# Performance work log

Hardware: AMD Instinct MI355X
Metric: run time of the kernel (lower is better)

The kernel has to match this reference:

```python
import jax, jax.numpy as jnp
import numpy as np

K_NEIGHBORS = 16
HEADS = 4
BN_EPS = 1e-5


def _bn(x, p):
    # eval-mode BatchNorm; p is [4, C] = (gamma, beta, running_mean, running_var), x is [..., C]
    g, b, m, v = p[0], p[1], p[2], p[3]
    return (x - m) * (g / jnp.sqrt(v + BN_EPS)) + b


def setup_inputs() -> dict:
    key = jax.random.key(0)
    ks = jax.random.split(key, 16)
    B, C, H, W = 4, 192, 32, 32
    Hd = 384  # hidden_channels

    def bn_params(k, c):
        k1, k2, k3, k4 = jax.random.split(k, 4)
        gamma = 1.0 + 0.1 * jax.random.normal(k1, (c,), jnp.float32)
        beta = 0.1 * jax.random.normal(k2, (c,), jnp.float32)
        mean = 0.1 * jax.random.normal(k3, (c,), jnp.float32)
        var = jax.random.uniform(k4, (c,), jnp.float32, 0.5, 1.5)
        return jnp.stack([gamma, beta, mean, var])

    x = jax.random.normal(ks[0], (B, C, H, W), jnp.float32)
    W1 = 0.05 * jax.random.normal(ks[1], (C, C), jnp.float32)          # fc1 1x1 conv [out,in]
    b1 = 0.02 * jax.random.normal(ks[2], (C,), jnp.float32)
    bn1 = bn_params(ks[3], C)
    Wg = 0.05 * jax.random.normal(ks[4], (C, HEADS * Hd), jnp.float32)  # GATConv shared lin
    att_src = 0.1 * jax.random.normal(ks[5], (HEADS, Hd), jnp.float32)
    att_dst = 0.1 * jax.random.normal(ks[6], (HEADS, Hd), jnp.float32)
    bg = 0.02 * jax.random.normal(ks[7], (Hd,), jnp.float32)            # GATConv bias (concat=False)
    bng = bn_params(ks[8], Hd)
    W2 = 0.05 * jax.random.normal(ks[9], (C, Hd), jnp.float32)          # fc2 1x1 conv [out,in]
    b2 = 0.02 * jax.random.normal(ks[10], (C,), jnp.float32)
    bn2 = bn_params(ks[11], C)
    return {"x": x, "W1": W1, "b1": b1, "bn1": bn1, "Wg": Wg,
            "att_src": att_src, "att_dst": att_dst, "bg": bg, "bng": bng,
            "W2": W2, "b2": b2, "bn2": bn2}


def reference(x, W1, b1, bn1, Wg, att_src, att_dst, bg, bng, W2, b2, bn2):
    B, C, H, W = x.shape
    N = H * W
    Hd = Wg.shape[1] // HEADS
    xf = x.reshape(B, C, N).transpose(0, 2, 1)          # [B,N,C] node features
    shortcut = xf

    # fc1: 1x1 conv + BN
    y = _bn(xf @ W1.T + b1, bn1)                        # [B,N,C]

    # dynamic KNN graph per image (loop=True -> self included, distance 0)
    sq = jnp.sum(y * y, axis=-1)                        # [B,N]
    dist = sq[:, :, None] + sq[:, None, :] - 2.0 * jnp.einsum('bnc,bmc->bnm', y, y)
    idx = jax.lax.top_k(-dist, K_NEIGHBORS)[1]          # [B,N,k] neighbor (source) ids
    bidx = jnp.arange(B)[:, None, None]

    # GATConv (shared lin, heads=4, concat=False -> mean over heads)
    h = (y @ Wg).reshape(B, N, HEADS, Hd)               # [B,N,h,d]
    a_src = jnp.sum(h * att_src, axis=-1)               # [B,N,h]
    a_dst = jnp.sum(h * att_dst, axis=-1)               # [B,N,h]
    e = jax.nn.leaky_relu(a_src[bidx, idx] + a_dst[:, :, None, :], 0.2)  # [B,N,k,h]
    attn = jax.nn.softmax(e, axis=2)                    # softmax over the k incoming edges
    h_nbr = h[bidx, idx]                                # [B,N,k,h,d] gathered neighbor feats
    g = jnp.einsum('bnkh,bnkhd->bnhd', attn, h_nbr).mean(axis=2) + bg  # [B,N,Hd]

    g = jax.nn.gelu(_bn(g, bng), approximate=False)

    # fc2: 1x1 conv + BN, residual
    out = _bn(g @ W2.T + b2, bn2) + shortcut            # [B,N,C]
    return out.transpose(0, 2, 1).reshape(B, C, H, W)
```

## Files before the change

### kernel.cpp

```cpp
#include <hip/hip_runtime.h>
#include <math.h>

#define Bb 4
#define Cc 192
#define NN 1024
#define HD 384
#define NH 4
#define FF 1536
#define KN 16
#define BN_EPS 1e-5f

typedef __attribute__((ext_vector_type(8))) short bf16x8;
typedef __attribute__((ext_vector_type(4))) float f32x4;

__device__ inline float b2f(ushort u) {
  return __uint_as_float(((unsigned)u) << 16);
}
__device__ inline ushort f2b(float f) {
  unsigned v = __float_as_uint(f);
  return (ushort)((v + 0x7fffu + ((v >> 16) & 1u)) >> 16);
}

#define FMA_ROW(ACC, AV, B) \
  ACC.x = fmaf(AV, B.x, ACC.x); ACC.y = fmaf(AV, B.y, ACC.y); \
  ACC.z = fmaf(AV, B.z, ACC.z); ACC.w = fmaf(AV, B.w, ACC.w);

__global__ __launch_bounds__(256) void k_prep(
    const float* __restrict__ W1, const float* __restrict__ W2,
    const float* __restrict__ Wg, float* __restrict__ W1T,
    float* __restrict__ W2T, ushort* __restrict__ WgTb) {
  __shared__ float tile[32][33];
  int id = blockIdx.x;
  const float* in; int R, C, cx, cy;
  float* outf = nullptr; ushort* outb = nullptr;
  if (id < 36)       { in = W1; R = Cc; C = Cc;   cx = id % 6;        cy = id / 6;        outf = W1T; }
  else if (id < 108) { int q = id - 36;  in = W2; R = Cc; C = HD;  cx = q % 12; cy = q / 12; outf = W2T; }
  else               { int q = id - 108; in = Wg; R = Cc; C = FF;  cx = q % 48; cy = q / 48; outb = WgTb; }
  int c0 = cx * 32, r0 = cy * 32;
  int tx = threadIdx.x & 31, ty = threadIdx.x >> 5;
#pragma unroll
  for (int i = 0; i < 4; ++i) {
    int r = ty + i * 8;
    tile[r][tx] = in[(size_t)(r0 + r) * C + c0 + tx];
  }
  __syncthreads();
#pragma unroll
  for (int i = 0; i < 4; ++i) {
    int r = ty + i * 8;
    float v = tile[tx][r];
    if (outf) outf[(size_t)(c0 + r) * R + r0 + tx] = v;
    else      outb[(size_t)(c0 + r) * R + r0 + tx] = f2b(v);
  }
}

__global__ __launch_bounds__(256) void k_fc1(
    const float* __restrict__ x, const float* __restrict__ W1T,
    const float* __restrict__ b1, const float* __restrict__ bn1,
    float* __restrict__ y, ushort* __restrict__ yb) {
  int nt = blockIdx.x, ct = blockIdx.y, b = blockIdx.z;
  int n0 = nt * 64, ct64 = ct * 64;
  __shared__ float As[64][64];
  __shared__ float Bs[64][64];
  int t = threadIdx.x;
  int tx = t & 15, ty = t >> 4;
  float4 acc[4];
#pragma unroll
  for (int i = 0; i < 4; ++i) acc[i] = {0.f, 0.f, 0.f, 0.f};
  for (int k0 = 0; k0 < Cc; k0 += 64) {
    __syncthreads();
#pragma unroll
    for (int i = 0; i < 4; ++i) {
      int fi = i * 256 + t;
      int r = fi >> 4, q = fi & 15;
      *(float4*)&As[r][q * 4] =
          *(const float4*)&x[((size_t)b * Cc + k0 + r) * NN + n0 + q * 4];
      *(float4*)&Bs[r][q * 4] =
          *(const float4*)&W1T[(size_t)(k0 + r) * Cc + ct64 + q * 4];
    }
    __syncthreads();
#pragma unroll 8
    for (int k = 0; k < 64; ++k) {
      float4 a = *(const float4*)&As[k][ty * 4];
      float4 bv = *(const float4*)&Bs[k][tx * 4];
      FMA_ROW(acc[0], a.x, bv)
      FMA_ROW(acc[1], a.y, bv)
      FMA_ROW(acc[2], a.z, bv)
      FMA_ROW(acc[3], a.w, bv)
    }
  }
  float s[4], mm[4], be[4], bias[4];
#pragma unroll
  for (int jj = 0; jj < 4; ++jj) {
    int c = ct64 + tx * 4 + jj;
    s[jj]    = bn1[c] / sqrtf(bn1[3 * Cc + c] + BN_EPS);
    mm[jj]   = bn1[2 * Cc + c];
    be[jj]   = bn1[Cc + c];
    bias[jj] = b1[c];
  }
  float accm[4][4] = {
      {acc[0].x, acc[0].y, acc[0].z, acc[0].w},
      {acc[1].x, acc[1].y, acc[1].z, acc[1].w},
      {acc[2].x, acc[2].y, acc[2].z, acc[2].w},
      {acc[3].x, acc[3].y, acc[3].z, acc[3].w}};
#pragma unroll
  for (int ii = 0; ii < 4; ++ii) {
    int n = n0 + ty * 4 + ii;
    float4 o;
    o.x = (accm[ii][0] + bias[0] - mm[0]) * s[0] + be[0];
    o.y = (accm[ii][1] + bias[1] - mm[1]) * s[1] + be[1];
    o.z = (accm[ii][2] + bias[2] - mm[2]) * s[2] + be[2];
    o.w = (accm[ii][3] + bias[3] - mm[3]) * s[3] + be[3];
    *(float4*)&y[((size_t)b * NN + n) * Cc + ct64 + tx * 4] = o;
    ushort4 ob = {f2b(o.x), f2b(o.y), f2b(o.z), f2b(o.w)};
    *(ushort4*)&yb[((size_t)b * NN + n) * Cc + ct64 + tx * 4] = ob;
  }
}

__global__ __launch_bounds__(256) void k_tr(const float* __restrict__ in,
                                            float* __restrict__ out,
                                            int R, int C) {
  __shared__ float tile[32][33];
  int c0 = blockIdx.x * 32, r0 = blockIdx.y * 32;
  const float* ip = in + (size_t)blockIdx.z * R * C;
  float* op = out + (size_t)blockIdx.z * R * C;
  int tx = threadIdx.x & 31, ty = threadIdx.x >> 5;
#pragma unroll
  for (int i = 0; i < 4; ++i) {
    int r = ty + i * 8;
    tile[r][tx] = ip[(size_t)(r0 + r) * C + c0 + tx];
  }
  __syncthreads();
#pragma unroll
  for (int i = 0; i < 4; ++i) {
    int r = ty + i * 8;
    op[(size_t)(c0 + r) * R + r0 + tx] = tile[tx][r];
  }
}

__global__ __launch_bounds__(64) void k_sq(const float* __restrict__ y,
                                           float* __restrict__ sq) {
  int bn = blockIdx.x;
  int lane = threadIdx.x;
  const float* yp = y + (size_t)bn * Cc;
  float s = 0.f;
  for (int k = lane; k < Cc; k += 64) { float v = yp[k]; s = fmaf(v, v, s); }
#pragma unroll
  for (int off = 32; off; off >>= 1) s += __shfl_down(s, off);
  if (lane == 0) sq[bn] = s;
}

__global__ __launch_bounds__(256) void k_hgemm_mfma(
    const ushort* __restrict__ yb, const ushort* __restrict__ WgTb,
    ushort* __restrict__ hb) {
  int r0 = blockIdx.x * 128, c0 = blockIdx.y * 128;
  __shared__ ushort Al[128][72];
  __shared__ ushort Bl[128][72];
  int t = threadIdx.x;
  int w = t >> 6, l = t & 63;
  int wr = w >> 1, wc = w & 1;
  f32x4 acc[4][4];
#pragma unroll
  for (int mt = 0; mt < 4; ++mt)
#pragma unroll
    for (int nt = 0; nt < 4; ++nt) acc[mt][nt] = {0.f, 0.f, 0.f, 0.f};
  for (int k0 = 0; k0 < Cc; k0 += 64) {
    __syncthreads();
#pragma unroll
    for (int i = 0; i < 4; ++i) {
      int u = i * 256 + t;
      int r = u >> 3, ko = (u & 7) * 8;
      *(int4*)&Al[r][ko] = *(const int4*)&yb[(size_t)(r0 + r) * Cc + k0 + ko];
      *(int4*)&Bl[r][ko] = *(const int4*)&WgTb[(size_t)(c0 + r) * Cc + k0 + ko];
    }
    __syncthreads();
#pragma unroll
    for (int ks = 0; ks < 2; ++ks) {
      bf16x8 af[4], bfr[4];
#pragma unroll
      for (int mt = 0; mt < 4; ++mt)
        af[mt] = *(const bf16x8*)&Al[wr * 64 + mt * 16 + (l & 15)][ks * 32 + (l >> 4) * 8];
#pragma unroll
      for (int nt = 0; nt < 4; ++nt)
        bfr[nt] = *(const bf16x8*)&Bl[wc * 64 + nt * 16 + (l & 15)][ks * 32 + (l >> 4) * 8];
#pragma unroll
      for (int mt = 0; mt < 4; ++mt)
#pragma unroll
        for (int nt = 0; nt < 4; ++nt)
          acc[mt][nt] = __builtin_amdgcn_mfma_f32_16x16x32_bf16(
              af[mt], bfr[nt], acc[mt][nt], 0, 0, 0);
    }
  }
  int col_l = l & 15, rg = l >> 4;
#pragma unroll
  for (int mt = 0; mt < 4; ++mt)
#pragma unroll
    for (int nt = 0; nt < 4; ++nt) {
      int col = c0 + wc * 64 + nt * 16 + col_l;
#pragma unroll
      for (int j = 0; j < 4; ++j) {
        int row = r0 + wr * 64 + mt * 16 + rg * 4 + j;
        hb[(size_t)row * FF + col] = f2b(acc[mt][nt][j]);
      }
    }
}

__global__ __launch_bounds__(256) void k_attn_coef(
    const ushort* __restrict__ hb, const float* __restrict__ att_src,
    const float* __restrict__ att_dst, float* __restrict__ asrc,
    float* __restrict__ adst) {
  int bn = blockIdx.x;
  int head = threadIdx.x / 64, lane = threadIdx.x % 64;
  const ushort* hp = hb + (size_t)bn * FF + head * HD;
  const float* as = att_src + head * HD;
  const float* ad = att_dst + head * HD;
  float s1 = 0.f, s2 = 0.f;
  for (int d = lane; d < HD; d += 64) {
    float v = b2f(hp[d]);
    s1 = fmaf(v, as[d], s1);
    s2 = fmaf(v, ad[d], s2);
  }
#pragma unroll
  for (int off = 32; off; off >>= 1) {
    s1 += __shfl_down(s1, off);
    s2 += __shfl_down(s2, off);
  }
  if (lane == 0) {
    asrc[bn * NH + head] = s1;
    adst[bn * NH + head] = s2;
  }
}

__global__ __launch_bounds__(256) void k_dist(const float* __restrict__ yT,
                                              const float* __restrict__ sq,
                                              float* __restrict__ dist) {
  int b = blockIdx.z;
  int n0 = blockIdx.y * 128, m0 = blockIdx.x * 64;
  __shared__ float As[64][128];
  __shared__ float Bs[64][64];
  const float* ytb = yT + (size_t)b * Cc * NN;
  int t = threadIdx.x;
  int tx = t & 15, ty = t >> 4;
  float4 acc[8];
#pragma unroll
  for (int i = 0; i < 8; ++i) acc[i] = {0.f, 0.f, 0.f, 0.f};
  for (int k0 = 0; k0 < Cc; k0 += 64) {
    __syncthreads();
#pragma unroll
    for (int i = 0; i < 8; ++i) {
      int fi = i * 256 + t;
      int kk = fi >> 5, n4 = fi & 31;
      *(float4*)&As[kk][n4 * 4] =
          *(const float4*)&ytb[(size_t)(k0 + kk) * NN + n0 + n4 * 4];
    }
#pragma unroll
    for (int i = 0; i < 4; ++i) {
      int fi = i * 256 + t;
      int kk = fi >> 4, m4 = fi & 15;
      *(float4*)&Bs[kk][m4 * 4] =
          *(const float4*)&ytb[(size_t)(k0 + kk) * NN + m0 + m4 * 4];
    }
    __syncthreads();
#pragma unroll 8
    for (int k = 0; k < 64; ++k) {
      float4 a0 = *(const float4*)&As[k][ty * 4];
      float4 a1 = *(const float4*)&As[k][64 + ty * 4];
      float4 b4 = *(const float4*)&Bs[k][tx * 4];
      FMA_ROW(acc[0], a0.x, b4)
      FMA_ROW(acc[1], a0.y, b4)
      FMA_ROW(acc[2], a0.z, b4)
      FMA_ROW(acc[3], a0.w, b4)
      FMA_ROW(acc[4], a1.x, b4)
      FMA_ROW(acc[5], a1.y, b4)
      FMA_ROW(acc[6], a1.z, b4)
      FMA_ROW(acc[7], a1.w, b4)
    }
  }
#pragma unroll
  for (int ii = 0; ii < 8; ++ii) {
    int n = n0 + ((ii < 4) ? (ty * 4 + ii) : (64 + ty * 4 + ii - 4));
    float sn = sq[b * NN + n];
    int mbase = m0 + tx * 4;
    float av[4] = {acc[ii].x, acc[ii].y, acc[ii].z, acc[ii].w};
    float4 o;
    o.x = sn + sq[b * NN + mbase + 0] - 2.f * av[0];
    o.y = sn + sq[b * NN + mbase + 1] - 2.f * av[1];
    o.z = sn + sq[b * NN + mbase + 2] - 2.f * av[2];
    o.w = sn + sq[b * NN + mbase + 3] - 2.f * av[3];
    *(float4*)&dist[((size_t)b * NN + n) * NN + mbase] = o;
  }
}

__global__ __launch_bounds__(64) void k_topk(const float* __restrict__ dist,
                                             int* __restrict__ idx) {
  int bn = blockIdx.x;
  int lane = threadIdx.x;
  const float4* dp = (const float4*)(dist + (size_t)bn * NN);
  float dv[16];
#pragma unroll
  for (int q = 0; q < 4; ++q) {
    float4 v = dp[lane + 64 * q];
    dv[q * 4 + 0] = v.x; dv[q * 4 + 1] = v.y;
    dv[q * 4 + 2] = v.z; dv[q * 4 + 3] = v.w;
  }
  for (int sel = 0; sel < KN; ++sel) {
    float bv = INFINITY;
    int bi = 0x7fffffff;
#pragma unroll
    for (int q = 0; q < 4; ++q)
#pragma unroll
      for (int j = 0; j < 4; ++j) {
        int m = (lane + 64 * q) * 4 + j;
        float v = dv[q * 4 + j];
        if (v < bv || (v == bv && m < bi)) { bv = v; bi = m; }
      }
#pragma unroll
    for (int off = 32; off; off >>= 1) {
      float ov = __shfl_xor(bv, off);
      int oi   = __shfl_xor(bi, off);
      if (ov < bv || (ov == bv && oi < bi)) { bv = ov; bi = oi; }
    }
    if (lane == 0) idx[bn * KN + sel] = bi;
#pragma unroll
    for (int q = 0; q < 4; ++q)
#pragma unroll
      for (int j = 0; j < 4; ++j)
        if ((lane + 64 * q) * 4 + j == bi) dv[q * 4 + j] = INFINITY;
  }
}

__global__ __launch_bounds__(128, 4) void k_gat(
    const ushort* __restrict__ hb, const float* __restrict__ asrc,
    const float* __restrict__ adst, const int* __restrict__ idx,
    const float* __restrict__ bg, const float* __restrict__ bng,
    float* __restrict__ g) {
  int bid = blockIdx.x;
  int bn = (bid & 7) * (Bb * NN / 8) + (bid >> 3);
  int b = bn / NN;
  __shared__ int nb[KN];
  __shared__ float attn[KN][NH];
  int t = threadIdx.x;
  if (t < KN) nb[t] = idx[bn * KN + t];
  __syncthreads();
  if (t < KN * NH) {
    int k = t % KN, hd = t / KN;
    float e = asrc[((size_t)b * NN + nb[k]) * NH + hd] +
              adst[(size_t)bn * NH + hd];
    e = (e >= 0.f) ? e : 0.2f * e;
    attn[k][hd] = e;
  }
  __syncthreads();
  if (t < NH) {
    float mx = -INFINITY;
    for (int k = 0; k < KN; ++k) mx = fmaxf(mx, attn[k][t]);
    float s = 0.f;
    for (int k = 0; k < KN; ++k) {
      float ev = expf(attn[k][t] - mx);
      attn[k][t] = ev;
      s += ev;
    }
    float inv = 1.f / s;
    for (int k = 0; k < KN; ++k) attn[k][t] *= inv;
  }
  __syncthreads();
  if (t < 96) {
    int d = t * 4;
    float4 acc = {0.f, 0.f, 0.f, 0.f};
#pragma unroll 4
    for (int k = 0; k < KN; ++k) {
      const ushort* hp = hb + ((size_t)b * NN + nb[k]) * FF + d;
      float4 aw = *(const float4*)&attn[k][0];
      ushort4 u0 = *(const ushort4*)&hp[0];
      ushort4 u1 = *(const ushort4*)&hp[HD];
      ushort4 u2 = *(const ushort4*)&hp[2 * HD];
      ushort4 u3 = *(const ushort4*)&hp[3 * HD];
      float4 h0 = {b2f(u0.x), b2f(u0.y), b2f(u0.z), b2f(u0.w)};
      float4 h1 = {b2f(u1.x), b2f(u1.y), b2f(u1.z), b2f(u1.w)};
      float4 h2 = {b2f(u2.x), b2f(u2.y), b2f(u2.z), b2f(u2.w)};
      float4 h3 = {b2f(u3.x), b2f(u3.y), b2f(u3.z), b2f(u3.w)};
      acc.x = fmaf(aw.x, h0.x, acc.x); acc.x = fmaf(aw.y, h1.x, acc.x);
      acc.x = fmaf(aw.z, h2.x, acc.x); acc.x = fmaf(aw.w, h3.x, acc.x);
      acc.y = fmaf(aw.x, h0.y, acc.y); acc.y = fmaf(aw.y, h1.y, acc.y);
      acc.y = fmaf(aw.z, h2.y, acc.y); acc.y = fmaf(aw.w, h3.y, acc.y);
      acc.z = fmaf(aw.x, h0.z, acc.z); acc.z = fmaf(aw.y, h1.z, acc.z);
      acc.z = fmaf(aw.z, h2.z, acc.z); acc.z = fmaf(aw.w, h3.z, acc.z);
      acc.w = fmaf(aw.x, h0.w, acc.w); acc.w = fmaf(aw.y, h1.w, acc.w);
      acc.w = fmaf(aw.z, h2.w, acc.w); acc.w = fmaf(aw.w, h3.w, acc.w);
    }
    float o[4] = {acc.x, acc.y, acc.z, acc.w};
    float4 r;
    float* rp = (float*)&r;
#pragma unroll
    for (int j = 0; j < 4; ++j) {
      int dd = d + j;
      float val = o[j] * 0.25f + bg[dd];
      float sc = bng[dd] / sqrtf(bng[3 * HD + dd] + BN_EPS);
      val = (val - bng[2 * HD + dd]) * sc + bng[HD + dd];
      val = 0.5f * val * (1.f + erff(val * 0.7071067811865475f));
      rp[j] = val;
    }
    *(float4*)&g[(size_t)bn * HD + d] = r;
  }
}

__global__ __launch_bounds__(256) void k_fc2(
    const float* __restrict__ gT, const float* __restrict__ W2T,
    const float* __restrict__ b2, const float* __restrict__ bn2,
    const float* __restrict__ x, float* __restrict__ out) {
  int nt = blockIdx.x, ct = blockIdx.y, b = blockIdx.z;
  int n0 = nt * 64, c0 = ct * 64;
  __shared__ float As[64][64];
  __shared__ float Bs[64][64];
  int t = threadIdx.x;
  int tx = t & 15, ty = t >> 4;
  float4 acc[4];
#pragma unroll
  for (int i = 0; i < 4; ++i) acc[i] = {0.f, 0.f, 0.f, 0.f};
  for (int k0 = 0; k0 < HD; k0 += 64) {
    __syncthreads();
#pragma unroll
    for (int i = 0; i < 4; ++i) {
      int fi = i * 256 + t;
      int r = fi >> 4, q = fi & 15;
      *(float4*)&As[r][q * 4] =
          *(const float4*)&gT[((size_t)b * HD + k0 + r) * NN + n0 + q * 4];
      *(float4*)&Bs[r][q * 4] =
          *(const float4*)&W2T[(size_t)(k0 + r) * Cc + c0 + q * 4];
    }
    __syncthreads();
#pragma unroll 8
    for (int k = 0; k < 64; ++k) {
      float4 a = *(const float4*)&As[k][ty * 4];
      float4 bv = *(const float4*)&Bs[k][tx * 4];
      FMA_ROW(acc[0], a.x, bv)
      FMA_ROW(acc[1], a.y, bv)
      FMA_ROW(acc[2], a.z, bv)
      FMA_ROW(acc[3], a.w, bv)
    }
  }
  float accm[4][4] = {
      {acc[0].x, acc[0].y, acc[0].z, acc[0].w},
      {acc[1].x, acc[1].y, acc[1].z, acc[1].w},
      {acc[2].x, acc[2].y, acc[2].z, acc[2].w},
      {acc[3].x, acc[3].y, acc[3].z, acc[3].w}};
#pragma unroll
  for (int jj = 0; jj < 4; ++jj) {
    int c = c0 + tx * 4 + jj;
    float s  = bn2[c] / sqrtf(bn2[3 * Cc + c] + BN_EPS);
    float mm = bn2[2 * Cc + c];
    float be = bn2[Cc + c];
    float bias = b2[c];
    float4 res = *(const float4*)&x[((size_t)b * Cc + c) * NN + n0 + ty * 4];
    float4 o;
    o.x = (accm[0][jj] + bias - mm) * s + be + res.x;
    o.y = (accm[1][jj] + bias - mm) * s + be + res.y;
    o.z = (accm[2][jj] + bias - mm) * s + be + res.z;
    o.w = (accm[3][jj] + bias - mm) * s + be + res.w;
    *(float4*)&out[((size_t)b * Cc + c) * NN + n0 + ty * 4] = o;
  }
}

extern "C" void kernel_launch(void* const* d_in, const int* in_sizes, int n_in,
                              void* d_out, int out_size, void* d_ws, size_t ws_size,
                              hipStream_t stream) {
  const float* x       = (const float*)d_in[0];
  const float* W1      = (const float*)d_in[1];
  const float* b1      = (const float*)d_in[2];
  const float* bn1     = (const float*)d_in[3];
  const float* Wg      = (const float*)d_in[4];
  const float* att_src = (const float*)d_in[5];
  const float* att_dst = (const float*)d_in[6];
  const float* bg      = (const float*)d_in[7];
  const float* bng     = (const float*)d_in[8];
  const float* W2      = (const float*)d_in[9];
  const float* b2      = (const float*)d_in[10];
  const float* bn2     = (const float*)d_in[11];
  float* out = (float*)d_out;

  float* ws    = (float*)d_ws;
  float* y     = ws;
  float* sq    = y + 786432;
  float* asrc  = sq + 4096;
  float* adst  = asrc + 16384;
  float* dist  = adst + 16384;
  float* g     = dist;
  int*   idx   = (int*)(dist + 4194304);
  float* yT    = dist + 4194304 + 65536;
  float* gT    = yT + 786432;
  float* W1T   = gT + 1572864;
  float* W2T   = W1T + 36864;
  ushort* yb   = (ushort*)(W2T + 73728);
  ushort* WgTb = (ushort*)(W2T + 73728 + 393216);
  ushort* hb   = (ushort*)(W2T + 73728 + 393216 + 147456);

  k_prep<<<396, 256, 0, stream>>>(W1, W2, Wg, W1T, W2T, WgTb);
  k_fc1<<<dim3(16, 3, 4), 256, 0, stream>>>(x, W1T, b1, bn1, y, yb);
  k_tr<<<dim3(6, 32, 4), 256, 0, stream>>>(y, yT, NN, Cc);
  k_sq<<<Bb * NN, 64, 0, stream>>>(y, sq);
  k_hgemm_mfma<<<dim3(32, 12), 256, 0, stream>>>(yb, WgTb, hb);
  k_attn_coef<<<Bb * NN, 256, 0, stream>>>(hb, att_src, att_dst, asrc, adst);
  k_dist<<<dim3(16, 8, 4), 256, 0, stream>>>(yT, sq, dist);
  k_topk<<<Bb * NN, 64, 0, stream>>>(dist, idx);
  k_gat<<<Bb * NN, 128, 0, stream>>>(hb, asrc, adst, idx, bg, bng, g);
  k_tr<<<dim3(12, 32, 4), 256, 0, stream>>>(g, gT, NN, HD);
  k_fc2<<<dim3(16, 3, 4), 256, 0, stream>>>(gT, W2T, b2, bn2, x, out);
}
```

Measured before the change: 148.2 us.

## Fold attention vectors into weights, run fc2 on MFMA, drop g transpose

New measurement: 160.4 us. +8.2%, slower.

```diff
diff --git a/kernel.cpp b/kernel.cpp
--- a/kernel.cpp
+++ b/kernel.cpp
@@ -27,29 +27,47 @@
 
 __global__ __launch_bounds__(256) void k_prep(
     const float* __restrict__ W1, const float* __restrict__ W2,
-    const float* __restrict__ Wg, float* __restrict__ W1T,
-    float* __restrict__ W2T, ushort* __restrict__ WgTb) {
+    const float* __restrict__ Wg, const float* __restrict__ att_src,
+    const float* __restrict__ att_dst, float* __restrict__ W1T,
+    ushort* __restrict__ W2b, ushort* __restrict__ WgTb,
+    float* __restrict__ Asml) {
   __shared__ float tile[32][33];
   int id = blockIdx.x;
-  const float* in; int R, C, cx, cy;
-  float* outf = nullptr; ushort* outb = nullptr;
-  if (id < 36)       { in = W1; R = Cc; C = Cc;   cx = id % 6;        cy = id / 6;        outf = W1T; }
-  else if (id < 108) { int q = id - 36;  in = W2; R = Cc; C = HD;  cx = q % 12; cy = q / 12; outf = W2T; }
-  else               { int q = id - 108; in = Wg; R = Cc; C = FF;  cx = q % 48; cy = q / 48; outb = WgTb; }
-  int c0 = cx * 32, r0 = cy * 32;
-  int tx = threadIdx.x & 31, ty = threadIdx.x >> 5;
-#pragma unroll
-  for (int i = 0; i < 4; ++i) {
-    int r = ty + i * 8;
-    tile[r][tx] = in[(size_t)(r0 + r) * C + c0 + tx];
-  }
-  __syncthreads();
-#pragma unroll
-  for (int i = 0; i < 4; ++i) {
-    int r = ty + i * 8;
-    float v = tile[tx][r];
-    if (outf) outf[(size_t)(c0 + r) * R + r0 + tx] = v;
-    else      outb[(size_t)(c0 + r) * R + r0 + tx] = f2b(v);
+  int t = threadIdx.x;
+  if (id < 36 || (id >= 108 && id < 396)) {
+    const float* in; int R, C, cx, cy;
+    float* outf = nullptr; ushort* outb = nullptr;
+    if (id < 36) { in = W1; R = Cc; C = Cc; cx = id % 6; cy = id / 6; outf = W1T; }
+    else { int q = id - 108; in = Wg; R = Cc; C = FF; cx = q % 48; cy = q / 48; outb = WgTb; }
+    int c0 = cx * 32, r0 = cy * 32;
+    int tx = t & 31, ty = t >> 5;
+#pragma unroll
+    for (int i = 0; i < 4; ++i) {
+      int r = ty + i * 8;
+      tile[r][tx] = in[(size_t)(r0 + r) * C + c0 + tx];
+    }
+    __syncthreads();
+#pragma unroll
+    for (int i = 0; i < 4; ++i) {
+      int r = ty + i * 8;
+      float v = tile[tx][r];
+      if (outf) outf[(size_t)(c0 + r) * R + r0 + tx] = v;
+      else      outb[(size_t)(c0 + r) * R + r0 + tx] = f2b(v);
+    }
+  } else if (id < 108) {
+    int base = (id - 36) * 1024 + t * 4;
+    float4 v = *(const float4*)&W2[base];
+    ushort4 o = {f2b(v.x), f2b(v.y), f2b(v.z), f2b(v.w)};
+    *(ushort4*)&W2b[base] = o;
+  } else {
+    int gi = (id - 396) * 256 + t;
+    int k = gi >> 3, j = gi & 7;
+    int h = j & 3;
+    const float* av = (j < 4) ? att_src : att_dst;
+    float acc = 0.f;
+    for (int d = 0; d < HD; ++d)
+      acc = fmaf(Wg[(size_t)k * FF + h * HD + d], av[h * HD + d], acc);
+    Asml[k * 8 + j] = acc;
   }
 }
 
@@ -204,30 +222,25 @@
     }
 }
 
-__global__ __launch_bounds__(256) void k_attn_coef(
-    const ushort* __restrict__ hb, const float* __restrict__ att_src,
-    const float* __restrict__ att_dst, float* __restrict__ asrc,
-    float* __restrict__ adst) {
-  int bn = blockIdx.x;
-  int head = threadIdx.x / 64, lane = threadIdx.x % 64;
-  const ushort* hp = hb + (size_t)bn * FF + head * HD;
-  const float* as = att_src + head * HD;
-  const float* ad = att_dst + head * HD;
-  float s1 = 0.f, s2 = 0.f;
-  for (int d = lane; d < HD; d += 64) {
-    float v = b2f(hp[d]);
-    s1 = fmaf(v, as[d], s1);
-    s2 = fmaf(v, ad[d], s2);
-  }
-#pragma unroll
-  for (int off = 32; off; off >>= 1) {
-    s1 += __shfl_down(s1, off);
-    s2 += __shfl_down(s2, off);
-  }
-  if (lane == 0) {
-    asrc[bn * NH + head] = s1;
-    adst[bn * NH + head] = s2;
-  }
+__global__ __launch_bounds__(256) void k_attn2(
+    const float* __restrict__ yT, const float* __restrict__ Asml,
+    float* __restrict__ asrc, float* __restrict__ adst) {
+  __shared__ float As[Cc][8];
+  int t = threadIdx.x;
+  for (int i = t; i < Cc * 8; i += 256) As[i >> 3][i & 7] = Asml[i];
+  int blk = blockIdx.x;
+  int b = blk >> 5;
+  int n0 = (blk & 31) * 32;
+  int nl = t & 31, j = t >> 5;
+  __syncthreads();
+  const float* yp = yT + (size_t)b * Cc * NN + n0 + nl;
+  float acc = 0.f;
+#pragma unroll 4
+  for (int k = 0; k < Cc; ++k)
+    acc = fmaf(yp[(size_t)k * NN], As[k][j], acc);
+  int bn = b * NN + n0 + nl;
+  if (j < 4) asrc[bn * NH + j] = acc;
+  else       adst[bn * NH + (j - 4)] = acc;
 }
 
 __global__ __launch_bounds__(256) void k_dist(const float* __restrict__ yT,
@@ -332,7 +345,7 @@
     const ushort* __restrict__ hb, const float* __restrict__ asrc,
     const float* __restrict__ adst, const int* __restrict__ idx,
     const float* __restrict__ bg, const float* __restrict__ bng,
-    float* __restrict__ g) {
+    ushort* __restrict__ gb) {
   int bid = blockIdx.x;
   int bn = (bid & 7) * (Bb * NN / 8) + (bid >> 3);
   int b = bn / NN;
@@ -387,8 +400,8 @@
       acc.w = fmaf(aw.z, h2.w, acc.w); acc.w = fmaf(aw.w, h3.w, acc.w);
     }
     float o[4] = {acc.x, acc.y, acc.z, acc.w};
-    float4 r;
-    float* rp = (float*)&r;
+    ushort4 r;
+    ushort* rp = (ushort*)&r;
 #pragma unroll
     for (int j = 0; j < 4; ++j) {
       int dd = d + j;
@@ -396,66 +409,88 @@
       float sc = bng[dd] / sqrtf(bng[3 * HD + dd] + BN_EPS);
       val = (val - bng[2 * HD + dd]) * sc + bng[HD + dd];
       val = 0.5f * val * (1.f + erff(val * 0.7071067811865475f));
-      rp[j] = val;
-    }
-    *(float4*)&g[(size_t)bn * HD + d] = r;
-  }
-}
-
-__global__ __launch_bounds__(256) void k_fc2(
-    const float* __restrict__ gT, const float* __restrict__ W2T,
+      rp[j] = f2b(val);
+    }
+    *(ushort4*)&gb[(size_t)bn * HD + d] = r;
+  }
+}
+
+__global__ __launch_bounds__(256) void k_fc2_mfma(
+    const ushort* __restrict__ gb, const ushort* __restrict__ W2b,
     const float* __restrict__ b2, const float* __restrict__ bn2,
     const float* __restrict__ x, float* __restrict__ out) {
-  int nt = blockIdx.x, ct = blockIdx.y, b = blockIdx.z;
-  int n0 = nt * 64, c0 = ct * 64;
-  __shared__ float As[64][64];
-  __shared__ float Bs[64][64];
-  int t = threadIdx.x;
-  int tx = t & 15, ty = t >> 4;
-  float4 acc[4];
-#pragma unroll
-  for (int i = 0; i < 4; ++i) acc[i] = {0.f, 0.f, 0.f, 0.f};
+  int r0 = blockIdx.x * 64;
+  int c0 = blockIdx.y * 64;
+  int b = r0 >> 10, n0 = r0 & 1023;
+  __shared__ ushort smem[2 * 64 * 72];
+  ushort* Al = smem;
+  ushort* Bl = smem + 64 * 72;
+  int t = threadIdx.x;
+  int w = t >> 6, l = t & 63;
+  int wr = w >> 1, wc = w & 1;
+  f32x4 acc[2][2];
+#pragma unroll
+  for (int mt = 0; mt < 2; ++mt)
+#pragma unroll
+    for (int nt = 0; nt < 2; ++nt) acc[mt][nt] = {0.f, 0.f, 0.f, 0.f};
   for (int k0 = 0; k0 < HD; k0 += 64) {
     __syncthreads();
 #pragma unroll
-    for (int i = 0; i < 4; ++i) {
-      int fi = i * 256 + t;
-      int r = fi >> 4, q = fi & 15;
-      *(float4*)&As[r][q * 4] =
-          *(const float4*)&gT[((size_t)b * HD + k0 + r) * NN + n0 + q * 4];
-      *(float4*)&Bs[r][q * 4] =
-          *(const float4*)&W2T[(size_t)(k0 + r) * Cc + c0 + q * 4];
-    }
-    __syncthreads();
-#pragma unroll 8
-    for (int k = 0; k < 64; ++k) {
-      float4 a = *(const float4*)&As[k][ty * 4];
-      float4 bv = *(const float4*)&Bs[k][tx * 4];
-      FMA_ROW(acc[0], a.x, bv)
-      FMA_ROW(acc[1], a.y, bv)
-      FMA_ROW(acc[2], a.z, bv)
-      FMA_ROW(acc[3], a.w, bv)
-    }
-  }
-  float accm[4][4] = {
-      {acc[0].x, acc[0].y, acc[0].z, acc[0].w},
-      {acc[1].x, acc[1].y, acc[1].z, acc[1].w},
-      {acc[2].x, acc[2].y, acc[2].z, acc[2].w},
-      {acc[3].x, acc[3].y, acc[3].z, acc[3].w}};
-#pragma unroll
-  for (int jj = 0; jj < 4; ++jj) {
-    int c = c0 + tx * 4 + jj;
+    for (int i = 0; i < 2; ++i) {
+      int u = i * 256 + t;
+      int r = u >> 3, ko = (u & 7) * 8;
+      *(int4*)&Al[r * 72 + ko] = *(const int4*)&gb[(size_t)(r0 + r) * HD + k0 + ko];
+      *(int4*)&Bl[r * 72 + ko] = *(const int4*)&W2b[(size_t)(c0 + r) * HD + k0 + ko];
+    }
+    __syncthreads();
+#pragma unroll
+    for (int ks = 0; ks < 2; ++ks) {
+      bf16x8 af[2], bfr[2];
+#pragma unroll
+      for (int mt = 0; mt < 2; ++mt)
+        af[mt] = *(const bf16x8*)&Al[(wr * 32 + mt * 16 + (l & 15)) * 72 + ks * 32 + (l >> 4) * 8];
+#pragma unroll
+      for (int nt = 0; nt < 2; ++nt)
+        bfr[nt] = *(const bf16x8*)&Bl[(wc * 32 + nt * 16 + (l & 15)) * 72 + ks * 32 + (l >> 4) * 8];
+#pragma unroll
+      for (int mt = 0; mt < 2; ++mt)
+#pragma unroll
+        for (int nt = 0; nt < 2; ++nt)
+          acc[mt][nt] = __builtin_amdgcn_mfma_f32_16x16x32_bf16(
+              af[mt], bfr[nt], acc[mt][nt], 0, 0, 0);
+    }
+  }
+  __syncthreads();
+  float* ct = (float*)smem;
+  int col_l = l & 15, rg = l >> 4;
+#pragma unroll
+  for (int mt = 0; mt < 2; ++mt)
+#pragma unroll
+    for (int nt = 0; nt < 2; ++nt) {
+      int cl = wc * 32 + nt * 16 + col_l;
+      int nl = wr * 32 + mt * 16 + rg * 4;
+      float4 v = {acc[mt][nt][0], acc[mt][nt][1], acc[mt][nt][2], acc[mt][nt][3]};
+      *(float4*)&ct[cl * 68 + nl] = v;
+    }
+  __syncthreads();
+#pragma unroll
+  for (int i = 0; i < 4; ++i) {
+    int u = i * 256 + t;
+    int cl = u >> 4, q = u & 15;
+    float4 v = *(const float4*)&ct[cl * 68 + q * 4];
+    int c = c0 + cl;
     float s  = bn2[c] / sqrtf(bn2[3 * Cc + c] + BN_EPS);
     float mm = bn2[2 * Cc + c];
     float be = bn2[Cc + c];
     float bias = b2[c];
-    float4 res = *(const float4*)&x[((size_t)b * Cc + c) * NN + n0 + ty * 4];
+    size_t base = ((size_t)b * Cc + c) * NN + n0 + q * 4;
+    float4 res = *(const float4*)&x[base];
     float4 o;
-    o.x = (accm[0][jj] + bias - mm) * s + be + res.x;
-    o.y = (accm[1][jj] + bias - mm) * s + be + res.y;
-    o.z = (accm[2][jj] + bias - mm) * s + be + res.z;
-    o.w = (accm[3][jj] + bias - mm) * s + be + res.w;
-    *(float4*)&out[((size_t)b * Cc + c) * NN + n0 + ty * 4] = o;
+    o.x = (v.x + bias - mm) * s + be + res.x;
+    o.y = (v.y + bias - mm) * s + be + res.y;
+    o.z = (v.z + bias - mm) * s + be + res.z;
+    o.w = (v.w + bias - mm) * s + be + res.w;
+    *(float4*)&out[base] = o;
   }
 }
 
@@ -482,25 +517,24 @@
   float* asrc  = sq + 4096;
   float* adst  = asrc + 16384;
   float* dist  = adst + 16384;
-  float* g     = dist;
   int*   idx   = (int*)(dist + 4194304);
   float* yT    = dist + 4194304 + 65536;
-  float* gT    = yT + 786432;
-  float* W1T   = gT + 1572864;
-  float* W2T   = W1T + 36864;
-  ushort* yb   = (ushort*)(W2T + 73728);
-  ushort* WgTb = (ushort*)(W2T + 73728 + 393216);
-  ushort* hb   = (ushort*)(W2T + 73728 + 393216 + 147456);
-
-  k_prep<<<396, 256, 0, stream>>>(W1, W2, Wg, W1T, W2T, WgTb);
+  float* W1T   = yT + 786432;
+  float* Asml  = W1T + 36864;
+  ushort* yb   = (ushort*)(Asml + 1536);
+  ushort* WgTb = yb + 786432;
+  ushort* hb   = WgTb + 294912;
+  ushort* gb   = hb + 6291456;
+  ushort* W2b  = gb + 1572864;
+
+  k_prep<<<402, 256, 0, stream>>>(W1, W2, Wg, att_src, att_dst, W1T, W2b, WgTb, Asml);
   k_fc1<<<dim3(16, 3, 4), 256, 0, stream>>>(x, W1T, b1, bn1, y, yb);
   k_tr<<<dim3(6, 32, 4), 256, 0, stream>>>(y, yT, NN, Cc);
   k_sq<<<Bb * NN, 64, 0, stream>>>(y, sq);
   k_hgemm_mfma<<<dim3(32, 12), 256, 0, stream>>>(yb, WgTb, hb);
-  k_attn_coef<<<Bb * NN, 256, 0, stream>>>(hb, att_src, att_dst, asrc, adst);
+  k_attn2<<<128, 256, 0, stream>>>(yT, Asml, asrc, adst);
   k_dist<<<dim3(16, 8, 4), 256, 0, stream>>>(yT, sq, dist);
   k_topk<<<Bb * NN, 64, 0, stream>>>(dist, idx);
-  k_gat<<<Bb * NN, 128, 0, stream>>>(hb, asrc, adst, idx, bg, bng, g);
-  k_tr<<<dim3(12, 32, 4), 256, 0, stream>>>(g, gT, NN, HD);
-  k_fc2<<<dim3(16, 3, 4), 256, 0, stream>>>(gT, W2T, b2, bn2, x, out);
-}
+  k_gat<<<Bb * NN, 128, 0, stream>>>(hb, asrc, adst, idx, bg, bng, gb);
+  k_fc2_mfma<<<dim3(64, 3), 256, 0, stream>>>(gb, W2b, b2, bn2, x, out);
+}
```
